# Kernel tuning notes

Measured on AMD Instinct MI355X. Metric: run time of the kernel, lower is better.

## Reference

```python
import jax, jax.numpy as jnp
import numpy as np

B, DIM, EMBDIM = 32, 512, 512
MEMSIZE, MEMSEQ = 32, 64
VOCAB = 50257


def setup_inputs() -> dict:
    key = jax.random.key(0)
    ks = jax.random.split(key, 10)
    inp = {
        'enc': jax.random.normal(ks[0], (B, DIM), jnp.float32),
        'encsumm': jax.random.normal(ks[1], (B, DIM), jnp.float32),
        'embsumm': jax.random.normal(ks[2], (B, EMBDIM), jnp.float32),
        'memencs': jax.random.normal(ks[3], (B, MEMSIZE, MEMSEQ, DIM), jnp.float32),
        'memencsumm': jax.random.normal(ks[4], (B, MEMSIZE, MEMSEQ, DIM), jnp.float32),
        'memembsumm': jax.random.normal(ks[5], (B, MEMSIZE, MEMSEQ, EMBDIM), jnp.float32),
        'memmask': jnp.ones((B, MEMSIZE, MEMSEQ), jnp.float32),
        'memids': jax.random.randint(ks[6], (B, MEMSIZE, MEMSEQ), 0, VOCAB, jnp.int64 if jax.config.jax_enable_x64 else jnp.int32),
        'W_out': jax.random.normal(ks[7], (VOCAB, 2 * DIM), jnp.float32) * 0.02,
        'b_out': jnp.zeros((VOCAB,), jnp.float32),
        'W_mix': jax.random.normal(ks[8], (2, 2 * DIM), jnp.float32) * 0.02,
        'b_mix': jnp.zeros((2,), jnp.float32),
        'unktok_mask': jnp.ones((VOCAB,), jnp.float32),  # no unktoks
    }
    return inp


def reference(enc, encsumm, embsumm, memencs, memencsumm, memembsumm, memmask,
              memids, W_out, b_out, W_mix, b_mix, unktok_mask):
    # copy branch: attention over flattened memory, scatter-add into vocab
    query = jnp.concatenate([embsumm, jnp.zeros_like(encsumm), enc], axis=-1)        # (B, 2*dim+embdim)
    keys = jnp.concatenate([memembsumm, jnp.zeros_like(memencsumm), memencs], axis=-1)  # (B, M, Z, 2*dim+embdim)
    w = jnp.einsum('bd,bmzd->bmz', query, keys) + jnp.log(memmask)
    b = w.shape[0]
    w = w.reshape(b, -1)                                    # (B, M*Z)
    alphas = jax.nn.softmax(w, axis=-1)
    mem_flat = memencs.reshape(b, -1, memencs.shape[-1])    # (B, M*Z, dim)
    mem_enc_summ = jnp.einsum('bm,bmd->bd', alphas, mem_flat)
    toks = memids.reshape(b, -1)                            # (B, M*Z)
    rows = jnp.arange(b)[:, None]
    vocsize = W_out.shape[0]
    probs_mem = jnp.zeros((b, vocsize), alphas.dtype).at[rows, toks].add(alphas)
    # generation branch
    h = jnp.concatenate([encsumm, enc], axis=-1)            # (B, 2*dim)
    logits_gen = h @ W_out.T + b_out + jnp.log(unktok_mask)[None, :]
    probs_gen = jax.nn.softmax(logits_gen, axis=-1)
    # mixer combine
    mix = jax.nn.softmax(h @ W_mix.T + b_mix, axis=-1)      # (B, 2)
    probs = mix[:, 0:1] * probs_gen + mix[:, 1:2] * probs_mem
    # original stack/gather trick: selects probs where nonzero, zeros where zero -> identity
    probs = jnp.where(probs != 0, probs, jnp.zeros_like(probs))
    return probs, mem_enc_summ
```

## Files before the change

kernel.cpp:

```cpp
#include <hip/hip_runtime.h>
#include <hip/hip_bf16.h>

#define NB   32
#define DIMK 512
#define MM   32
#define ZZ   64
#define MZV  2048
#define VOC  50257

typedef __attribute__((ext_vector_type(8))) short  short8;
typedef __attribute__((ext_vector_type(4))) float  f32x4;
typedef __attribute__((ext_vector_type(8))) unsigned short ushort8;

#define WS_W      0
#define WS_PVEC   (WS_W + NB*MZV)
#define WS_LSTAT  (WS_PVEC + NB*MM*DIMK)
#define WS_GSTATW (WS_LSTAT + NB*MM*2)
#define WS_MIX    (WS_GSTATW + NB*2)
#define WS_GPART  (WS_MIX + NB*2)
#define WS_H      (WS_GPART + NB*32*2)

__device__ __forceinline__ ushort8 cvt8(float4 a, float4 b) {
    union { ushort8 u; __hip_bfloat162 h[4]; } r;
    r.h[0] = __float22bfloat162_rn(make_float2(a.x, a.y));
    r.h[1] = __float22bfloat162_rn(make_float2(a.z, a.w));
    r.h[2] = __float22bfloat162_rn(make_float2(b.x, b.y));
    r.h[3] = __float22bfloat162_rn(make_float2(b.z, b.w));
    return r.u;
}

__global__ void k0_stageh(const float* __restrict__ encsumm, const float* __restrict__ enc,
                          float* __restrict__ ws)
{
    int b = blockIdx.x;
    int c = threadIdx.x * 4;
    const float* src = (c < DIMK) ? (encsumm + b*DIMK + c) : (enc + b*DIMK + (c - DIMK));
    float4 v = *(const float4*)src;
    union { ushort4 u; __hip_bfloat162 h[2]; } o;
    o.h[0] = __float22bfloat162_rn(make_float2(v.x, v.y));
    o.h[1] = __float22bfloat162_rn(make_float2(v.z, v.w));
    *(ushort4*)((unsigned short*)(ws + WS_H) + b*1024 + c) = o.u;
}

__global__ __launch_bounds__(256) void k1_mem(
    const float* __restrict__ enc, const float* __restrict__ embsumm,
    const float* __restrict__ memencs, const float* __restrict__ memembsumm,
    const float* __restrict__ memmask, float* __restrict__ ws)
{
    int blk = blockIdx.x;
    int b = blk >> 5, m = blk & 31;
    int tid = threadIdx.x, wid = tid >> 6, lane = tid & 63;
    int c0 = lane * 4, c1 = c0 + 256;
    const float* encb = enc + b * DIMK;
    const float* embb = embsumm + b * DIMK;
    float4 qe0 = *(const float4*)(encb + c0);
    float4 qe1 = *(const float4*)(encb + c1);
    float4 qm0 = *(const float4*)(embb + c0);
    float4 qm1 = *(const float4*)(embb + c1);
    const float* meb = memencs    + (long)(b*MM + m) * ZZ * DIMK;
    const float* mmb = memembsumm + (long)(b*MM + m) * ZZ * DIMK;
    const float* mkb = memmask    + (long)(b*MM + m) * ZZ;
    float* w_ws = ws + WS_W + b*MZV + m*ZZ;

    float lmax = -3.0e38f, lsum = 0.f;
    float4 a0 = make_float4(0.f,0.f,0.f,0.f), a1 = make_float4(0.f,0.f,0.f,0.f);

    for (int z = wid; z < ZZ; z += 4) {
        const float* mer = meb + z*DIMK;
        const float* mmr = mmb + z*DIMK;
        float4 e0 = *(const float4*)(mer + c0);
        float4 e1 = *(const float4*)(mer + c1);
        float4 s0 = *(const float4*)(mmr + c0);
        float4 s1 = *(const float4*)(mmr + c1);
        float d = e0.x*qe0.x + e0.y*qe0.y + e0.z*qe0.z + e0.w*qe0.w
                + e1.x*qe1.x + e1.y*qe1.y + e1.z*qe1.z + e1.w*qe1.w
                + s0.x*qm0.x + s0.y*qm0.y + s0.z*qm0.z + s0.w*qm0.w
                + s1.x*qm1.x + s1.y*qm1.y + s1.z*qm1.z + s1.w*qm1.w;
        #pragma unroll
        for (int off = 32; off; off >>= 1) d += __shfl_xor(d, off);
        d += logf(mkb[z]);
        if (lane == 0) w_ws[z] = d;
        float nm = fmaxf(lmax, d);
        float sc = __expf(lmax - nm);
        float e  = __expf(d - nm);
        lsum = lsum * sc + e;
        a0.x = a0.x*sc + e*e0.x; a0.y = a0.y*sc + e*e0.y;
        a0.z = a0.z*sc + e*e0.z; a0.w = a0.w*sc + e*e0.w;
        a1.x = a1.x*sc + e*e1.x; a1.y = a1.y*sc + e*e1.y;
        a1.z = a1.z*sc + e*e1.z; a1.w = a1.w*sc + e*e1.w;
        lmax = nm;
    }

    __shared__ float sacc[4][DIMK];
    __shared__ float sst[4][2];
    *(float4*)&sacc[wid][c0] = a0;
    *(float4*)&sacc[wid][c1] = a1;
    if (lane == 0) { sst[wid][0] = lmax; sst[wid][1] = lsum; }
    __syncthreads();
    float bm = fmaxf(fmaxf(sst[0][0], sst[1][0]), fmaxf(sst[2][0], sst[3][0]));
    float sc0 = __expf(sst[0][0]-bm), sc1 = __expf(sst[1][0]-bm);
    float sc2 = __expf(sst[2][0]-bm), sc3 = __expf(sst[3][0]-bm);
    float bs = sst[0][1]*sc0 + sst[1][1]*sc1 + sst[2][1]*sc2 + sst[3][1]*sc3;
    int d0 = tid * 2;
    float2 v0 = *(float2*)&sacc[0][d0];
    float2 v1 = *(float2*)&sacc[1][d0];
    float2 v2 = *(float2*)&sacc[2][d0];
    float2 v3 = *(float2*)&sacc[3][d0];
    float p0 = v0.x*sc0 + v1.x*sc1 + v2.x*sc2 + v3.x*sc3;
    float p1 = v0.y*sc0 + v1.y*sc1 + v2.y*sc2 + v3.y*sc3;
    float* pv = ws + WS_PVEC + (long)(b*MM+m)*DIMK + d0;
    pv[0] = p0; pv[1] = p1;
    if (tid == 0) { float* ls = ws + WS_LSTAT + (b*MM+m)*2; ls[0] = bm; ls[1] = bs; }
}

__global__ __launch_bounds__(256) void k2_comb(float* __restrict__ out, float* __restrict__ ws)
{
    int b = blockIdx.x, tid = threadIdx.x;
    const float* ls = ws + WS_LSTAT + b*MM*2;
    float gm = -3.0e38f;
    #pragma unroll
    for (int m = 0; m < MM; m++) gm = fmaxf(gm, ls[m*2]);
    float gs = 0.f;
    #pragma unroll
    for (int m = 0; m < MM; m++) gs += ls[m*2+1] * __expf(ls[m*2] - gm);
    if (tid == 0) { ws[WS_GSTATW + b*2] = gm; ws[WS_GSTATW + b*2 + 1] = gs; }
    float inv = 1.0f / gs;
    int d0 = tid * 2;
    float p0 = 0.f, p1 = 0.f;
    for (int m = 0; m < MM; m++) {
        float sc = __expf(ls[m*2] - gm);
        const float* pv = ws + WS_PVEC + (long)(b*MM+m)*DIMK + d0;
        p0 += pv[0]*sc; p1 += pv[1]*sc;
    }
    out[(long)NB*VOC + b*DIMK + d0]     = p0 * inv;
    out[(long)NB*VOC + b*DIMK + d0 + 1] = p1 * inv;
}

__global__ void k3_mix(const float* __restrict__ encsumm, const float* __restrict__ enc,
                       const float* __restrict__ W_mix, const float* __restrict__ b_mix,
                       float* __restrict__ ws)
{
    int b = blockIdx.x, l = threadIdx.x;
    float d0 = 0.f, d1 = 0.f;
    #pragma unroll
    for (int p = 0; p < 4; p++) {
        int cc = l*4 + p*256;
        float4 h4 = (cc < 512) ? *(const float4*)(encsumm + b*DIMK + cc)
                               : *(const float4*)(enc + b*DIMK + cc - 512);
        float4 w0 = *(const float4*)(W_mix + cc);
        float4 w1 = *(const float4*)(W_mix + 1024 + cc);
        d0 += h4.x*w0.x + h4.y*w0.y + h4.z*w0.z + h4.w*w0.w;
        d1 += h4.x*w1.x + h4.y*w1.y + h4.z*w1.z + h4.w*w1.w;
    }
    #pragma unroll
    for (int off = 32; off; off >>= 1) { d0 += __shfl_xor(d0, off); d1 += __shfl_xor(d1, off); }
    if (l == 0) {
        d0 += b_mix[0]; d1 += b_mix[1];
        float mx = fmaxf(d0, d1);
        float e0 = __expf(d0-mx), e1 = __expf(d1-mx);
        float s = e0 + e1;
        ws[WS_MIX + b*2] = e0/s; ws[WS_MIX + b*2 + 1] = e1/s;
    }
}

__global__ __launch_bounds__(256) void k4_gemm(
    const unsigned short* __restrict__ hbf,
    const float* __restrict__ W_out, const float* __restrict__ b_out,
    const float* __restrict__ unk, float* __restrict__ logits)
{
    __shared__ __align__(16) unsigned short b_lds[2][8*64*8];
    __shared__ __align__(16) unsigned short a_lds[2][8*32*8];
    int tid = threadIdx.x, wid = tid >> 6, lane = tid & 63;
    int vt = blockIdx.x * 64;

    int r = tid >> 2, q = tid & 3;
    long grow = min(vt + r, VOC - 1);
    const float* wbase = W_out + grow * 1024 + q * 16;
    int ar = tid >> 3, ag = tid & 7;
    const unsigned short* abase = hbf + ar * 1024 + ag * 8;

    int lg = lane >> 4, ln = lane & 15;
    int vrow = wid*16 + ln;

    f32x4 acc0 = {0.f,0.f,0.f,0.f};
    f32x4 acc1 = {0.f,0.f,0.f,0.f};
    float4 f0, f1, f2, f3; ushort8 av;

    int g0 = 2*q, g1 = 2*q + 1;
    int bw0 = (g0*64 + (r ^ ((g0 & 3) << 2))) * 8;
    int bw1 = (g1*64 + (r ^ ((g1 & 3) << 2))) * 8;
    int aw  = (ag*32 + (ar ^ ag)) * 8;

#define LOADC(c) do { const float* wp = wbase + (c)*64;              \
        f0 = *(const float4*)(wp);      f1 = *(const float4*)(wp+4); \
        f2 = *(const float4*)(wp+8);    f3 = *(const float4*)(wp+12);\
        av = *(const ushort8*)(abase + (c)*64); } while (0)
#define WRITEC(buf) do {                                \
        *(ushort8*)&b_lds[buf][bw0] = cvt8(f0, f1);     \
        *(ushort8*)&b_lds[buf][bw1] = cvt8(f2, f3);     \
        *(ushort8*)&a_lds[buf][aw]  = av; } while (0)

    LOADC(0); WRITEC(0);
    LOADC(1);
    __syncthreads();

    #pragma unroll 2
    for (int c = 0; c < 16; ++c) {
        int buf = c & 1;
        #pragma unroll
        for (int s = 0; s < 2; ++s) {
            int g = s*4 + lg;
            short8 bfrag = *(const short8*)&b_lds[buf][(g*64 + (vrow ^ ((g & 3) << 2)))*8];
            short8 a0 = *(const short8*)&a_lds[buf][(g*32 + (ln ^ g))*8];
            short8 a1 = *(const short8*)&a_lds[buf][(g*32 + ((ln + 16) ^ g))*8];
            acc0 = __builtin_amdgcn_mfma_f32_16x16x32_bf16(a0, bfrag, acc0, 0, 0, 0);
            acc1 = __builtin_amdgcn_mfma_f32_16x16x32_bf16(a1, bfrag, acc1, 0, 0, 0);
        }
        if (c < 15) {
            WRITEC(buf ^ 1);
            if (c < 14) LOADC(c + 2);
        }
        __syncthreads();
    }
#undef LOADC
#undef WRITEC

    int v = vt + vrow;
    if (v < VOC) {
        float bias = b_out[v] + logf(unk[v]);
        #pragma unroll
        for (int rr = 0; rr < 4; ++rr) {
            int m = lg*4 + rr;
            logits[(long)m*VOC + v]        = acc0[rr] + bias;
            logits[(long)(m+16)*VOC + v]   = acc1[rr] + bias;
        }
    }
}

__global__ __launch_bounds__(256) void k5_gstat(const float* __restrict__ logits, float* __restrict__ ws)
{
    int chunk = blockIdx.x, b = blockIdx.y, tid = threadIdx.x;
    const int CH = (VOC + 31) / 32;
    int v0 = chunk * CH;
    int v1 = min(VOC, v0 + CH);
    float m = -3.0e38f, s = 0.f;
    for (int v = v0 + tid; v < v1; v += 256) {
        float x = logits[(long)b*VOC + v];
        float nm = fmaxf(m, x);
        s = s*__expf(m - nm) + __expf(x - nm);
        m = nm;
    }
    #pragma unroll
    for (int off = 32; off; off >>= 1) {
        float om = __shfl_xor(m, off), os = __shfl_xor(s, off);
        float nm = fmaxf(m, om);
        s = s*__expf(m - nm) + os*__expf(om - nm);
        m = nm;
    }
    __shared__ float sm[4], ssum[4];
    int wid = tid >> 6, lane = tid & 63;
    if (lane == 0) { sm[wid] = m; ssum[wid] = s; }
    __syncthreads();
    if (tid == 0) {
        float gm = fmaxf(fmaxf(sm[0], sm[1]), fmaxf(sm[2], sm[3]));
        float gs = ssum[0]*__expf(sm[0]-gm) + ssum[1]*__expf(sm[1]-gm)
                 + ssum[2]*__expf(sm[2]-gm) + ssum[3]*__expf(sm[3]-gm);
        ws[WS_GPART + (b*32 + chunk)*2]     = gm;
        ws[WS_GPART + (b*32 + chunk)*2 + 1] = gs;
    }
}

__global__ __launch_bounds__(256) void k6_final(float* __restrict__ probs, const float* __restrict__ ws)
{
    int v = blockIdx.x*256 + threadIdx.x;
    int b = blockIdx.y;
    float gm = -3.0e38f;
    #pragma unroll
    for (int i = 0; i < 32; ++i) gm = fmaxf(gm, ws[WS_GPART + (b*32+i)*2]);
    float gs = 0.f;
    #pragma unroll
    for (int i = 0; i < 32; ++i)
        gs += ws[WS_GPART + (b*32+i)*2 + 1] * __expf(ws[WS_GPART + (b*32+i)*2] - gm);
    if (v >= VOC) return;
    float mix0 = ws[WS_MIX + b*2];
    long idx = (long)b*VOC + v;
    probs[idx] = mix0 * __expf(probs[idx] - gm) / gs;
}

__global__ __launch_bounds__(256) void k7_scatter(const int* __restrict__ memids,
                                                  const float* __restrict__ ws,
                                                  float* __restrict__ probs)
{
    int idx = blockIdx.x*256 + threadIdx.x;
    int b = idx >> 11, mz = idx & 2047;
    float gm = ws[WS_GSTATW + b*2], gs = ws[WS_GSTATW + b*2 + 1];
    float mix1 = ws[WS_MIX + b*2 + 1];
    float alpha = __expf(ws[WS_W + b*MZV + mz] - gm) / gs;
    int tok = memids[b*MZV + mz];
    atomicAdd(&probs[(long)b*VOC + tok], mix1 * alpha);
}

extern "C" void kernel_launch(void* const* d_in, const int* in_sizes, int n_in,
                              void* d_out, int out_size, void* d_ws, size_t ws_size,
                              hipStream_t stream)
{
    const float* enc        = (const float*)d_in[0];
    const float* encsumm    = (const float*)d_in[1];
    const float* embsumm    = (const float*)d_in[2];
    const float* memencs    = (const float*)d_in[3];
    const float* memembsumm = (const float*)d_in[5];
    const float* memmask    = (const float*)d_in[6];
    const int*   memids     = (const int*)d_in[7];
    const float* W_out      = (const float*)d_in[8];
    const float* b_out      = (const float*)d_in[9];
    const float* W_mix      = (const float*)d_in[10];
    const float* b_mix      = (const float*)d_in[11];
    const float* unk        = (const float*)d_in[12];
    float* out = (float*)d_out;
    float* ws  = (float*)d_ws;

    hipLaunchKernelGGL(k0_stageh, dim3(NB), dim3(256), 0, stream, encsumm, enc, ws);
    hipLaunchKernelGGL(k1_mem, dim3(NB*MM), dim3(256), 0, stream,
                       enc, embsumm, memencs, memembsumm, memmask, ws);
    hipLaunchKernelGGL(k2_comb, dim3(NB), dim3(256), 0, stream, out, ws);
    hipLaunchKernelGGL(k3_mix, dim3(NB), dim3(64), 0, stream, encsumm, enc, W_mix, b_mix, ws);
    hipLaunchKernelGGL(k4_gemm, dim3((VOC + 63)/64), dim3(256), 0, stream,
                       (const unsigned short*)(ws + WS_H), W_out, b_out, unk, out);
    hipLaunchKernelGGL(k5_gstat, dim3(32, NB), dim3(256), 0, stream, out, ws);
    hipLaunchKernelGGL(k6_final, dim3((VOC + 255)/256, NB), dim3(256), 0, stream, out, ws);
    hipLaunchKernelGGL(k7_scatter, dim3(NB*MZV/256), dim3(256), 0, stream, memids, ws, out);
}
```

Measured before the change: 138.1 us.

## Fuse mixer into combine kernel and deepen GEMM global-load prefetch

```diff
diff --git a/kernel.cpp b/kernel.cpp
--- a/kernel.cpp
+++ b/kernel.cpp
@@ -113,7 +113,10 @@
     if (tid == 0) { float* ls = ws + WS_LSTAT + (b*MM+m)*2; ls[0] = bm; ls[1] = bs; }
 }
 
-__global__ __launch_bounds__(256) void k2_comb(float* __restrict__ out, float* __restrict__ ws)
+__global__ __launch_bounds__(256) void k2_comb(
+    const float* __restrict__ encsumm, const float* __restrict__ enc,
+    const float* __restrict__ W_mix, const float* __restrict__ b_mix,
+    float* __restrict__ out, float* __restrict__ ws)
 {
     int b = blockIdx.x, tid = threadIdx.x;
     const float* ls = ws + WS_LSTAT + b*MM*2;
@@ -134,36 +137,33 @@
     }
     out[(long)NB*VOC + b*DIMK + d0]     = p0 * inv;
     out[(long)NB*VOC + b*DIMK + d0 + 1] = p1 * inv;
-}
-
-__global__ void k3_mix(const float* __restrict__ encsumm, const float* __restrict__ enc,
-                       const float* __restrict__ W_mix, const float* __restrict__ b_mix,
-                       float* __restrict__ ws)
-{
-    int b = blockIdx.x, l = threadIdx.x;
-    float d0 = 0.f, d1 = 0.f;
-    #pragma unroll
-    for (int p = 0; p < 4; p++) {
-        int cc = l*4 + p*256;
-        float4 h4 = (cc < 512) ? *(const float4*)(encsumm + b*DIMK + cc)
-                               : *(const float4*)(enc + b*DIMK + cc - 512);
-        float4 w0 = *(const float4*)(W_mix + cc);
-        float4 w1 = *(const float4*)(W_mix + 1024 + cc);
-        d0 += h4.x*w0.x + h4.y*w0.y + h4.z*w0.z + h4.w*w0.w;
-        d1 += h4.x*w1.x + h4.y*w1.y + h4.z*w1.z + h4.w*w1.w;
-    }
-    #pragma unroll
-    for (int off = 32; off; off >>= 1) { d0 += __shfl_xor(d0, off); d1 += __shfl_xor(d1, off); }
-    if (l == 0) {
-        d0 += b_mix[0]; d1 += b_mix[1];
-        float mx = fmaxf(d0, d1);
-        float e0 = __expf(d0-mx), e1 = __expf(d1-mx);
-        float s = e0 + e1;
-        ws[WS_MIX + b*2] = e0/s; ws[WS_MIX + b*2 + 1] = e1/s;
-    }
-}
-
-__global__ __launch_bounds__(256) void k4_gemm(
+
+    if (tid < 64) {
+        int l = tid;
+        float m0 = 0.f, m1 = 0.f;
+        #pragma unroll
+        for (int p = 0; p < 4; p++) {
+            int cc = l*4 + p*256;
+            float4 h4 = (cc < 512) ? *(const float4*)(encsumm + b*DIMK + cc)
+                                   : *(const float4*)(enc + b*DIMK + cc - 512);
+            float4 w0 = *(const float4*)(W_mix + cc);
+            float4 w1 = *(const float4*)(W_mix + 1024 + cc);
+            m0 += h4.x*w0.x + h4.y*w0.y + h4.z*w0.z + h4.w*w0.w;
+            m1 += h4.x*w1.x + h4.y*w1.y + h4.z*w1.z + h4.w*w1.w;
+        }
+        #pragma unroll
+        for (int off = 32; off; off >>= 1) { m0 += __shfl_xor(m0, off); m1 += __shfl_xor(m1, off); }
+        if (l == 0) {
+            m0 += b_mix[0]; m1 += b_mix[1];
+            float mx = fmaxf(m0, m1);
+            float e0 = __expf(m0-mx), e1 = __expf(m1-mx);
+            float s = e0 + e1;
+            ws[WS_MIX + b*2] = e0/s; ws[WS_MIX + b*2 + 1] = e1/s;
+        }
+    }
+}
+
+__global__ __launch_bounds__(256, 4) void k4_gemm(
     const unsigned short* __restrict__ hbf,
     const float* __restrict__ W_out, const float* __restrict__ b_out,
     const float* __restrict__ unk, float* __restrict__ logits)
@@ -184,46 +184,62 @@
 
     f32x4 acc0 = {0.f,0.f,0.f,0.f};
     f32x4 acc1 = {0.f,0.f,0.f,0.f};
-    float4 f0, f1, f2, f3; ushort8 av;
+    float4 Af0, Af1, Af2, Af3; ushort8 Aa;
+    float4 Bf0, Bf1, Bf2, Bf3; ushort8 Ba;
 
     int g0 = 2*q, g1 = 2*q + 1;
     int bw0 = (g0*64 + (r ^ ((g0 & 3) << 2))) * 8;
     int bw1 = (g1*64 + (r ^ ((g1 & 3) << 2))) * 8;
     int aw  = (ag*32 + (ar ^ ag)) * 8;
 
-#define LOADC(c) do { const float* wp = wbase + (c)*64;              \
-        f0 = *(const float4*)(wp);      f1 = *(const float4*)(wp+4); \
-        f2 = *(const float4*)(wp+8);    f3 = *(const float4*)(wp+12);\
-        av = *(const ushort8*)(abase + (c)*64); } while (0)
-#define WRITEC(buf) do {                                \
-        *(ushort8*)&b_lds[buf][bw0] = cvt8(f0, f1);     \
-        *(ushort8*)&b_lds[buf][bw1] = cvt8(f2, f3);     \
-        *(ushort8*)&a_lds[buf][aw]  = av; } while (0)
-
-    LOADC(0); WRITEC(0);
-    LOADC(1);
+#define LOAD_A(c) do { const float* wp = wbase + (c)*64;                 \
+        Af0 = *(const float4*)(wp);      Af1 = *(const float4*)(wp+4);   \
+        Af2 = *(const float4*)(wp+8);    Af3 = *(const float4*)(wp+12);  \
+        Aa  = *(const ushort8*)(abase + (c)*64); } while (0)
+#define LOAD_B(c) do { const float* wp = wbase + (c)*64;                 \
+        Bf0 = *(const float4*)(wp);      Bf1 = *(const float4*)(wp+4);   \
+        Bf2 = *(const float4*)(wp+8);    Bf3 = *(const float4*)(wp+12);  \
+        Ba  = *(const ushort8*)(abase + (c)*64); } while (0)
+#define WRITE_A(buf) do {                                \
+        *(ushort8*)&b_lds[buf][bw0] = cvt8(Af0, Af1);    \
+        *(ushort8*)&b_lds[buf][bw1] = cvt8(Af2, Af3);    \
+        *(ushort8*)&a_lds[buf][aw]  = Aa; } while (0)
+#define WRITE_B(buf) do {                                \
+        *(ushort8*)&b_lds[buf][bw0] = cvt8(Bf0, Bf1);    \
+        *(ushort8*)&b_lds[buf][bw1] = cvt8(Bf2, Bf3);    \
+        *(ushort8*)&a_lds[buf][aw]  = Ba; } while (0)
+#define COMPUTE(buf) do {                                                          \
+        _Pragma("unroll")                                                          \
+        for (int s = 0; s < 2; ++s) {                                              \
+            int g = s*4 + lg;                                                      \
+            short8 bfrag = *(const short8*)&b_lds[buf][(g*64 + (vrow ^ ((g&3)<<2)))*8]; \
+            short8 a0 = *(const short8*)&a_lds[buf][(g*32 + (ln ^ g))*8];          \
+            short8 a1 = *(const short8*)&a_lds[buf][(g*32 + ((ln + 16) ^ g))*8];   \
+            acc0 = __builtin_amdgcn_mfma_f32_16x16x32_bf16(a0, bfrag, acc0, 0, 0, 0); \
+            acc1 = __builtin_amdgcn_mfma_f32_16x16x32_bf16(a1, bfrag, acc1, 0, 0, 0); \
+        } } while (0)
+
+    LOAD_A(0); LOAD_B(1);
+    WRITE_A(0);
+    LOAD_A(2);
     __syncthreads();
 
-    #pragma unroll 2
-    for (int c = 0; c < 16; ++c) {
-        int buf = c & 1;
-        #pragma unroll
-        for (int s = 0; s < 2; ++s) {
-            int g = s*4 + lg;
-            short8 bfrag = *(const short8*)&b_lds[buf][(g*64 + (vrow ^ ((g & 3) << 2)))*8];
-            short8 a0 = *(const short8*)&a_lds[buf][(g*32 + (ln ^ g))*8];
-            short8 a1 = *(const short8*)&a_lds[buf][(g*32 + ((ln + 16) ^ g))*8];
-            acc0 = __builtin_amdgcn_mfma_f32_16x16x32_bf16(a0, bfrag, acc0, 0, 0, 0);
-            acc1 = __builtin_amdgcn_mfma_f32_16x16x32_bf16(a1, bfrag, acc1, 0, 0, 0);
-        }
-        if (c < 15) {
-            WRITEC(buf ^ 1);
-            if (c < 14) LOADC(c + 2);
-        }
+    for (int cc = 0; cc < 8; ++cc) {
+        int c0 = cc*2, c1 = c0 + 1;
+        if (cc >= 1 && c0 + 2 < 16) LOAD_A(c0 + 2);
+        COMPUTE(0);
+        WRITE_B(1);
         __syncthreads();
-    }
-#undef LOADC
-#undef WRITEC
+        if (c1 + 2 < 16) LOAD_B(c1 + 2);
+        COMPUTE(1);
+        if (c1 < 15) WRITE_A(0);
+        __syncthreads();
+    }
+#undef LOAD_A
+#undef LOAD_B
+#undef WRITE_A
+#undef WRITE_B
+#undef COMPUTE
 
     int v = vt + vrow;
     if (v < VOC) {
@@ -322,8 +338,8 @@
     hipLaunchKernelGGL(k0_stageh, dim3(NB), dim3(256), 0, stream, encsumm, enc, ws);
     hipLaunchKernelGGL(k1_mem, dim3(NB*MM), dim3(256), 0, stream,
                        enc, embsumm, memencs, memembsumm, memmask, ws);
-    hipLaunchKernelGGL(k2_comb, dim3(NB), dim3(256), 0, stream, out, ws);
-    hipLaunchKernelGGL(k3_mix, dim3(NB), dim3(64), 0, stream, encsumm, enc, W_mix, b_mix, ws);
+    hipLaunchKernelGGL(k2_comb, dim3(NB), dim3(256), 0, stream,
+                       encsumm, enc, W_mix, b_mix, out, ws);
     hipLaunchKernelGGL(k4_gemm, dim3((VOC + 63)/64), dim3(256), 0, stream,
                        (const unsigned short*)(ws + WS_H), W_out, b_out, unk, out);
     hipLaunchKernelGGL(k5_gstat, dim3(32, NB), dim3(256), 0, stream, out, ws);
```

After: 142.3 us. 1.03x slower.

## Shrink GEMM vocab tile to 32 rows and fold mixer into combine kernel

Applied to the files above, without the earlier changes.

```diff
diff --git a/kernel.cpp b/kernel.cpp
--- a/kernel.cpp
+++ b/kernel.cpp
@@ -113,7 +113,10 @@
     if (tid == 0) { float* ls = ws + WS_LSTAT + (b*MM+m)*2; ls[0] = bm; ls[1] = bs; }
 }
 
-__global__ __launch_bounds__(256) void k2_comb(float* __restrict__ out, float* __restrict__ ws)
+__global__ __launch_bounds__(256) void k2_comb(
+    const float* __restrict__ encsumm, const float* __restrict__ enc,
+    const float* __restrict__ W_mix, const float* __restrict__ b_mix,
+    float* __restrict__ out, float* __restrict__ ws)
 {
     int b = blockIdx.x, tid = threadIdx.x;
     const float* ls = ws + WS_LSTAT + b*MM*2;
@@ -134,87 +137,75 @@
     }
     out[(long)NB*VOC + b*DIMK + d0]     = p0 * inv;
     out[(long)NB*VOC + b*DIMK + d0 + 1] = p1 * inv;
-}
-
-__global__ void k3_mix(const float* __restrict__ encsumm, const float* __restrict__ enc,
-                       const float* __restrict__ W_mix, const float* __restrict__ b_mix,
-                       float* __restrict__ ws)
-{
-    int b = blockIdx.x, l = threadIdx.x;
-    float d0 = 0.f, d1 = 0.f;
-    #pragma unroll
-    for (int p = 0; p < 4; p++) {
-        int cc = l*4 + p*256;
-        float4 h4 = (cc < 512) ? *(const float4*)(encsumm + b*DIMK + cc)
-                               : *(const float4*)(enc + b*DIMK + cc - 512);
-        float4 w0 = *(const float4*)(W_mix + cc);
-        float4 w1 = *(const float4*)(W_mix + 1024 + cc);
-        d0 += h4.x*w0.x + h4.y*w0.y + h4.z*w0.z + h4.w*w0.w;
-        d1 += h4.x*w1.x + h4.y*w1.y + h4.z*w1.z + h4.w*w1.w;
-    }
-    #pragma unroll
-    for (int off = 32; off; off >>= 1) { d0 += __shfl_xor(d0, off); d1 += __shfl_xor(d1, off); }
-    if (l == 0) {
-        d0 += b_mix[0]; d1 += b_mix[1];
-        float mx = fmaxf(d0, d1);
-        float e0 = __expf(d0-mx), e1 = __expf(d1-mx);
-        float s = e0 + e1;
-        ws[WS_MIX + b*2] = e0/s; ws[WS_MIX + b*2 + 1] = e1/s;
-    }
-}
-
-__global__ __launch_bounds__(256) void k4_gemm(
+
+    if (tid < 64) {
+        int l = tid;
+        float m0 = 0.f, m1 = 0.f;
+        #pragma unroll
+        for (int p = 0; p < 4; p++) {
+            int cc = l*4 + p*256;
+            float4 h4 = (cc < 512) ? *(const float4*)(encsumm + b*DIMK + cc)
+                                   : *(const float4*)(enc + b*DIMK + cc - 512);
+            float4 w0 = *(const float4*)(W_mix + cc);
+            float4 w1 = *(const float4*)(W_mix + 1024 + cc);
+            m0 += h4.x*w0.x + h4.y*w0.y + h4.z*w0.z + h4.w*w0.w;
+            m1 += h4.x*w1.x + h4.y*w1.y + h4.z*w1.z + h4.w*w1.w;
+        }
+        #pragma unroll
+        for (int off = 32; off; off >>= 1) { m0 += __shfl_xor(m0, off); m1 += __shfl_xor(m1, off); }
+        if (l == 0) {
+            m0 += b_mix[0]; m1 += b_mix[1];
+            float mx = fmaxf(m0, m1);
+            float e0 = __expf(m0-mx), e1 = __expf(m1-mx);
+            float s = e0 + e1;
+            ws[WS_MIX + b*2] = e0/s; ws[WS_MIX + b*2 + 1] = e1/s;
+        }
+    }
+}
+
+__global__ __launch_bounds__(256, 6) void k4_gemm(
     const unsigned short* __restrict__ hbf,
     const float* __restrict__ W_out, const float* __restrict__ b_out,
     const float* __restrict__ unk, float* __restrict__ logits)
 {
-    __shared__ __align__(16) unsigned short b_lds[2][8*64*8];
+    __shared__ __align__(16) unsigned short b_lds[2][8*32*8];
     __shared__ __align__(16) unsigned short a_lds[2][8*32*8];
     int tid = threadIdx.x, wid = tid >> 6, lane = tid & 63;
-    int vt = blockIdx.x * 64;
-
-    int r = tid >> 2, q = tid & 3;
+    int wv = wid >> 1, wb = wid & 1;
+    int vt = blockIdx.x * 32;
+
+    int r = tid >> 3, gq = tid & 7;
     long grow = min(vt + r, VOC - 1);
-    const float* wbase = W_out + grow * 1024 + q * 16;
-    int ar = tid >> 3, ag = tid & 7;
-    const unsigned short* abase = hbf + ar * 1024 + ag * 8;
+    const float* wbase = W_out + grow * 1024 + gq * 8;
+    const unsigned short* abase = hbf + r * 1024 + gq * 8;
 
     int lg = lane >> 4, ln = lane & 15;
-    int vrow = wid*16 + ln;
-
-    f32x4 acc0 = {0.f,0.f,0.f,0.f};
-    f32x4 acc1 = {0.f,0.f,0.f,0.f};
-    float4 f0, f1, f2, f3; ushort8 av;
-
-    int g0 = 2*q, g1 = 2*q + 1;
-    int bw0 = (g0*64 + (r ^ ((g0 & 3) << 2))) * 8;
-    int bw1 = (g1*64 + (r ^ ((g1 & 3) << 2))) * 8;
-    int aw  = (ag*32 + (ar ^ ag)) * 8;
-
-#define LOADC(c) do { const float* wp = wbase + (c)*64;              \
-        f0 = *(const float4*)(wp);      f1 = *(const float4*)(wp+4); \
-        f2 = *(const float4*)(wp+8);    f3 = *(const float4*)(wp+12);\
+
+    f32x4 acc = {0.f,0.f,0.f,0.f};
+    float4 f0, f1; ushort8 av;
+
+    int bw = (gq*32 + (r ^ ((gq & 3) << 2))) * 8;
+    int aw = (gq*32 + (r ^ gq)) * 8;
+
+#define LOADC(c) do { const float* wp = wbase + (c)*64;            \
+        f0 = *(const float4*)(wp); f1 = *(const float4*)(wp+4);    \
         av = *(const ushort8*)(abase + (c)*64); } while (0)
-#define WRITEC(buf) do {                                \
-        *(ushort8*)&b_lds[buf][bw0] = cvt8(f0, f1);     \
-        *(ushort8*)&b_lds[buf][bw1] = cvt8(f2, f3);     \
-        *(ushort8*)&a_lds[buf][aw]  = av; } while (0)
+#define WRITEC(buf) do {                            \
+        *(ushort8*)&b_lds[buf][bw] = cvt8(f0, f1);  \
+        *(ushort8*)&a_lds[buf][aw] = av; } while (0)
 
     LOADC(0); WRITEC(0);
     LOADC(1);
     __syncthreads();
 
-    #pragma unroll 2
     for (int c = 0; c < 16; ++c) {
         int buf = c & 1;
         #pragma unroll
         for (int s = 0; s < 2; ++s) {
             int g = s*4 + lg;
-            short8 bfrag = *(const short8*)&b_lds[buf][(g*64 + (vrow ^ ((g & 3) << 2)))*8];
-            short8 a0 = *(const short8*)&a_lds[buf][(g*32 + (ln ^ g))*8];
-            short8 a1 = *(const short8*)&a_lds[buf][(g*32 + ((ln + 16) ^ g))*8];
-            acc0 = __builtin_amdgcn_mfma_f32_16x16x32_bf16(a0, bfrag, acc0, 0, 0, 0);
-            acc1 = __builtin_amdgcn_mfma_f32_16x16x32_bf16(a1, bfrag, acc1, 0, 0, 0);
+            short8 bfrag = *(const short8*)&b_lds[buf][(g*32 + ((wv*16 + ln) ^ ((g & 3) << 2)))*8];
+            short8 afrag = *(const short8*)&a_lds[buf][(g*32 + ((wb*16 + ln) ^ g))*8];
+            acc = __builtin_amdgcn_mfma_f32_16x16x32_bf16(afrag, bfrag, acc, 0, 0, 0);
         }
         if (c < 15) {
             WRITEC(buf ^ 1);
@@ -225,14 +216,13 @@
 #undef LOADC
 #undef WRITEC
 
-    int v = vt + vrow;
+    int v = vt + wv*16 + ln;
     if (v < VOC) {
         float bias = b_out[v] + logf(unk[v]);
         #pragma unroll
         for (int rr = 0; rr < 4; ++rr) {
-            int m = lg*4 + rr;
-            logits[(long)m*VOC + v]        = acc0[rr] + bias;
-            logits[(long)(m+16)*VOC + v]   = acc1[rr] + bias;
+            int m = wb*16 + lg*4 + rr;
+            logits[(long)m*VOC + v] = acc[rr] + bias;
         }
     }
 }
@@ -322,9 +312,9 @@
     hipLaunchKernelGGL(k0_stageh, dim3(NB), dim3(256), 0, stream, encsumm, enc, ws);
     hipLaunchKernelGGL(k1_mem, dim3(NB*MM), dim3(256), 0, stream,
                        enc, embsumm, memencs, memembsumm, memmask, ws);
-    hipLaunchKernelGGL(k2_comb, dim3(NB), dim3(256), 0, stream, out, ws);
-    hipLaunchKernelGGL(k3_mix, dim3(NB), dim3(64), 0, stream, encsumm, enc, W_mix, b_mix, ws);
-    hipLaunchKernelGGL(k4_gemm, dim3((VOC + 63)/64), dim3(256), 0, stream,
+    hipLaunchKernelGGL(k2_comb, dim3(NB), dim3(256), 0, stream,
+                       encsumm, enc, W_mix, b_mix, out, ws);
+    hipLaunchKernelGGL(k4_gemm, dim3((VOC + 31)/32), dim3(256), 0, stream,
                        (const unsigned short*)(ws + WS_H), W_out, b_out, unk, out);
     hipLaunchKernelGGL(k5_gstat, dim3(32, NB), dim3(256), 0, stream, out, ws);
     hipLaunchKernelGGL(k6_final, dim3((VOC + 255)/256, NB), dim3(256), 0, stream, out, ws);
```

Result: no change. 140.6 us (+1.8%).
